# Kernel optimization log

Hardware: AMD Instinct MI355X
Metric: run time of the kernel (lower is better)

The kernel has to match this reference:

```python
import jax, jax.numpy as jnp
import numpy as np

N_NODES = 100000
N_EDGES = 50000
NNZ = 1600000
IN_DIM, HID_DIM, N_CLASSES = 128, 128, 16


def setup_inputs() -> dict:
    key = jax.random.key(0)
    k1, k2, k3, k4, k5 = jax.random.split(key, 5)
    x = jax.random.normal(k1, (N_NODES, IN_DIM), dtype=jnp.float32)
    node_idx = jax.random.randint(k2, (NNZ,), 0, N_NODES, dtype=jnp.int64)
    edge_idx = jax.random.randint(k3, (NNZ,), 0, N_EDGES, dtype=jnp.int64)
    # glorot-ish weights, zero bias (PyG HypergraphConv: Linear(bias=False) + bias Parameter)
    W1 = jax.random.normal(k4, (IN_DIM, HID_DIM), dtype=jnp.float32) * (1.0 / np.sqrt(IN_DIM))
    b1 = jnp.zeros((HID_DIM,), dtype=jnp.float32)
    W2 = jax.random.normal(k5, (HID_DIM, N_CLASSES), dtype=jnp.float32) * (1.0 / np.sqrt(HID_DIM))
    b2 = jnp.zeros((N_CLASSES,), dtype=jnp.float32)
    return {"x": x, "node_idx": node_idx, "edge_idx": edge_idx, "num_edges": N_EDGES,
            "W1": W1, "b1": b1, "W2": W2, "b2": b2}


def hypergraph_conv(x, W, b, node_idx, edge_idx, num_edges):
    """PyG HypergraphConv (no attention, unit hyperedge weights):
       out = D^{-1} H B^{-1} H^T (x W) + b
    implemented as gather -> segment_sum (node->edge) -> gather -> segment_sum (edge->node)."""
    n_nodes = x.shape[0]
    ones = jnp.ones(node_idx.shape[0], dtype=x.dtype)
    deg = jax.ops.segment_sum(ones, node_idx, num_segments=n_nodes)      # D: node degree
    edeg = jax.ops.segment_sum(ones, edge_idx, num_segments=num_edges)   # B: hyperedge size
    Dinv = jnp.where(deg > 0, 1.0 / deg, 0.0)
    Binv = jnp.where(edeg > 0, 1.0 / edeg, 0.0)

    xw = x @ W                                                            # [N, F_out]
    # node -> hyperedge, norm = B^{-1} applied per message (indexed by edge)
    msg_ne = xw[node_idx] * Binv[edge_idx][:, None]                       # [nnz, F_out]
    e_feat = jax.ops.segment_sum(msg_ne, edge_idx, num_segments=num_edges)
    # hyperedge -> node, norm = D^{-1} applied per message (indexed by node)
    msg_en = e_feat[edge_idx] * Dinv[node_idx][:, None]                   # [nnz, F_out]
    out = jax.ops.segment_sum(msg_en, node_idx, num_segments=n_nodes)
    return out + b


def reference(x, node_idx, edge_idx, num_edges, W1, b1, W2, b2):
    # Dropout is inactive in eval mode; model is relu(conv1) -> conv2.
    h = jax.nn.relu(hypergraph_conv(x, W1, b1, node_idx, edge_idx, num_edges))
    return hypergraph_conv(h, W2, b2, node_idx, edge_idx, num_edges)
```

## Files before the change

kernel.cpp:

```cpp
#include <hip/hip_runtime.h>
#include <hip/hip_fp16.h>


#define N_EDGES_C 50000
#define F1 128
#define F2 16
#define CHUNK 4096
#define EBIN_SHIFT 7
#define NBIN_SHIFT 8
#define EBINS 391
#define NBINS 391

typedef __attribute__((ext_vector_type(8))) _Float16 half8;
typedef __attribute__((ext_vector_type(4))) float f32x4;
typedef unsigned short ushort16_t;


__global__ __launch_bounds__(256) void hist_chunk_kernel(
    const int* __restrict__ node_idx, const int* __restrict__ edge_idx,
    int* __restrict__ echunkcnt, int* __restrict__ nchunkcnt, int nnz) {
  __shared__ int ebc[EBINS], nbc[NBINS];
  const int t = threadIdx.x;
  for (int b = t; b < EBINS; b += 256) ebc[b] = 0;
  for (int b = t; b < NBINS; b += 256) nbc[b] = 0;
  __syncthreads();
  const int base = blockIdx.x * CHUNK;
  int end = base + CHUNK; if (end > nnz) end = nnz;
  for (int i = base + t; i < end; i += 256) {
    atomicAdd(&ebc[edge_idx[i] >> EBIN_SHIFT], 1);
    atomicAdd(&nbc[node_idx[i] >> NBIN_SHIFT], 1);
  }
  __syncthreads();
  const int nC = gridDim.x;
  for (int b = t; b < EBINS; b += 256) echunkcnt[b * nC + blockIdx.x] = ebc[b];
  for (int b = t; b < NBINS; b += 256) nchunkcnt[b * nC + blockIdx.x] = nbc[b];
}

__global__ __launch_bounds__(256) void cscan_p1_kernel(
    const int* __restrict__ ecc, const int* __restrict__ ncc,
    int* __restrict__ epart, int* __restrict__ npart,
    int Le, int Ln, int nbE) {
  __shared__ int red[256];
  const int t = threadIdx.x;
  const int b = blockIdx.x;
  const int* src; int L; int* dst; int bb;
  if (b < nbE) { src = ecc; L = Le; dst = epart; bb = b; }
  else         { src = ncc; L = Ln; dst = npart; bb = b - nbE; }
  int base = bb * 1024 + t * 4;
  int s = 0;
#pragma unroll
  for (int j = 0; j < 4; ++j) { int i = base + j; if (i < L) s += src[i]; }
  red[t] = s;
  __syncthreads();
  for (int d = 128; d > 0; d >>= 1) {
    if (t < d) red[t] += red[t + d];
    __syncthreads();
  }
  if (t == 0) dst[bb] = red[0];
}

__global__ __launch_bounds__(256) void cscan_p2_kernel(
    int* __restrict__ epart, int* __restrict__ npart,
    int* __restrict__ ebinbase, int* __restrict__ nbinbase,
    int nbE, int nbN, int nnz) {
  __shared__ int se[256], sn[256];
  const int t = threadIdx.x;
  se[t] = (t < nbE) ? epart[t] : 0;
  sn[t] = (t < nbN) ? npart[t] : 0;
  __syncthreads();
  for (int d = 1; d < 256; d <<= 1) {
    int ve = (t >= d) ? se[t - d] : 0;
    int vn = (t >= d) ? sn[t - d] : 0;
    __syncthreads();
    se[t] += ve; sn[t] += vn;
    __syncthreads();
  }
  if (t < nbE) epart[t] = (t > 0) ? se[t - 1] : 0;
  if (t < nbN) npart[t] = (t > 0) ? sn[t - 1] : 0;
  if (t == 0) { ebinbase[EBINS] = nnz; nbinbase[NBINS] = nnz; }
}

__global__ __launch_bounds__(256) void cscan_p3_kernel(
    const int* __restrict__ ecc, const int* __restrict__ ncc,
    const int* __restrict__ epart, const int* __restrict__ npart,
    int* __restrict__ erunoff, int* __restrict__ nrunoff,
    int* __restrict__ ebinbase, int* __restrict__ nbinbase,
    int Le, int Ln, int nbE, int nC) {
  __shared__ int red[256];
  const int t = threadIdx.x;
  const int b = blockIdx.x;
  const int* src; const int* part; int L; int* ro; int* bba; int bb;
  if (b < nbE) { src = ecc; part = epart; L = Le; ro = erunoff; bba = ebinbase; bb = b; }
  else         { src = ncc; part = npart; L = Ln; ro = nrunoff; bba = nbinbase; bb = b - nbE; }
  int base = bb * 1024 + t * 4;
  int v[4]; int s = 0;
#pragma unroll
  for (int j = 0; j < 4; ++j) { int i = base + j; v[j] = (i < L) ? src[i] : 0; s += v[j]; }
  red[t] = s;
  __syncthreads();
  for (int d = 1; d < 256; d <<= 1) {
    int x = (t >= d) ? red[t - d] : 0;
    __syncthreads();
    red[t] += x;
    __syncthreads();
  }
  int run = part[bb] + ((t > 0) ? red[t - 1] : 0);
#pragma unroll
  for (int j = 0; j < 4; ++j) {
    int i = base + j;
    if (i < L) {
      ro[i] = run;
      if (i % nC == 0) bba[i / nC] = run;
      run += v[j];
    }
  }
}


__global__ __launch_bounds__(256) void stage_kernel(
    const int* __restrict__ node_idx, const int* __restrict__ edge_idx,
    const int* __restrict__ erunoff, const int* __restrict__ nrunoff,
    unsigned* __restrict__ epairs, unsigned* __restrict__ npairs, int nnz) {
  __shared__ int ecur[EBINS], ncur[NBINS];
  const int t = threadIdx.x;
  const int nC = gridDim.x;
  for (int b = t; b < EBINS; b += 256) ecur[b] = erunoff[b * nC + blockIdx.x];
  for (int b = t; b < NBINS; b += 256) ncur[b] = nrunoff[b * nC + blockIdx.x];
  __syncthreads();
  const int base = blockIdx.x * CHUNK;
  int end = base + CHUNK; if (end > nnz) end = nnz;
  for (int i = base + t; i < end; i += 256) {
    int e = edge_idx[i];
    int n = node_idx[i];
    int p = atomicAdd(&ecur[e >> EBIN_SHIFT], 1);
    epairs[p] = ((unsigned)n << 7) | (unsigned)(e & 127);
    int q = atomicAdd(&ncur[n >> NBIN_SHIFT], 1);
    npairs[q] = ((unsigned)e << 8) | (unsigned)(n & 255);
  }
}

__global__ __launch_bounds__(256) void bin_scatter_kernel(
    const unsigned* __restrict__ epairs, const unsigned* __restrict__ npairs,
    const int* __restrict__ ebinbase, const int* __restrict__ nbinbase,
    int* __restrict__ eoff, int* __restrict__ noff,
    int* __restrict__ enbr, ushort16_t* __restrict__ nnbr,
    int n_edges, int n_nodes) {
  __shared__ int cnt[256];
  __shared__ int scn[256];
  const int bid = blockIdx.x;
  const int t = threadIdx.x;
  if (bid < EBINS) {
    const int e0 = bid << EBIN_SHIFT;
    const int ne = min(1 << EBIN_SHIFT, n_edges - e0);
    const int beg = ebinbase[bid], end = ebinbase[bid + 1];
    if (t < 128) cnt[t] = 0;
    __syncthreads();
    for (int j = beg + t; j < end; j += 256) atomicAdd(&cnt[epairs[j] & 127u], 1);
    __syncthreads();
    if (t < 128) scn[t] = cnt[t];
    __syncthreads();
    for (int d = 1; d < 128; d <<= 1) {
      int x = 0;
      if (t < 128 && t >= d) x = scn[t - d];
      __syncthreads();
      if (t < 128) scn[t] += x;
      __syncthreads();
    }
    int pos0 = 0;
    if (t < 128) {
      int excl = (t > 0) ? scn[t - 1] : 0;
      pos0 = beg + excl;
      if (t < ne) eoff[e0 + t] = pos0;
    }
    __syncthreads();
    if (t < 128) scn[t] = pos0;
    __syncthreads();
    for (int j = beg + t; j < end; j += 256) {
      unsigned p = epairs[j];
      int pos = atomicAdd(&scn[p & 127u], 1);
      enbr[pos] = (int)(p >> 7);
    }
    if (bid == EBINS - 1 && t == 0) eoff[n_edges] = end;
  } else {
    const int b = bid - EBINS;
    const int n0 = b << NBIN_SHIFT;
    const int nn = min(1 << NBIN_SHIFT, n_nodes - n0);
    const int beg = nbinbase[b], end = nbinbase[b + 1];
    cnt[t] = 0;
    __syncthreads();
    for (int j = beg + t; j < end; j += 256) atomicAdd(&cnt[npairs[j] & 255u], 1);
    __syncthreads();
    scn[t] = cnt[t];
    __syncthreads();
    for (int d = 1; d < 256; d <<= 1) {
      int x = (t >= d) ? scn[t - d] : 0;
      __syncthreads();
      scn[t] += x;
      __syncthreads();
    }
    int excl = (t > 0) ? scn[t - 1] : 0;
    int pos0 = beg + excl;
    if (t < nn) noff[n0 + t] = pos0;
    __syncthreads();
    scn[t] = pos0;
    __syncthreads();
    for (int j = beg + t; j < end; j += 256) {
      unsigned p = npairs[j];
      int pos = atomicAdd(&scn[p & 255u], 1);
      nnbr[pos] = (ushort16_t)(p >> 8);
    }
    if (bid == EBINS + NBINS - 1 && t == 0) noff[n_nodes] = end;
  }
}


__global__ __launch_bounds__(256) void w1t_kernel(
    const float* __restrict__ W1, __half* __restrict__ W1t) {
  int i = blockIdx.x * 256 + threadIdx.x;
  int n = i >> 7, k = i & 127;
  W1t[i] = __float2half(W1[k * 128 + n]);
}


__global__ __launch_bounds__(256) void gemm1_kernel(
    const float* __restrict__ A, const __half* __restrict__ W1t16,
    __half* __restrict__ C16, int M) {
  __shared__ _Float16 As[64 * 136];
  __shared__ _Float16 Bs[128 * 136];
  const int t = threadIdx.x;
  const int bm = blockIdx.x * 64;

#pragma unroll
  for (int i = 0; i < 8; ++i) {
    int lin = i * 256 + t;
    int row = lin >> 5;
    int c4 = lin & 31;
    int grow = bm + row;
    float4 v = make_float4(0.f, 0.f, 0.f, 0.f);
    if (grow < M) v = *(const float4*)(A + (size_t)grow * 128 + c4 * 4);
    _Float16* dst = &As[row * 136 + c4 * 4];
    dst[0] = (_Float16)v.x; dst[1] = (_Float16)v.y;
    dst[2] = (_Float16)v.z; dst[3] = (_Float16)v.w;
  }
#pragma unroll
  for (int i = 0; i < 8; ++i) {
    int lin = i * 256 + t;
    int n = lin >> 4;
    int c = lin & 15;
    *(float4*)&Bs[n * 136 + c * 8] = *(const float4*)(W1t16 + n * 128 + c * 8);
  }
  __syncthreads();

  const int w = t >> 6;
  const int lane = t & 63;
  const int l16 = lane & 15;
  const int quad = lane >> 4;

  f32x4 acc[8];
#pragma unroll
  for (int n = 0; n < 8; ++n) acc[n] = (f32x4){0.f, 0.f, 0.f, 0.f};

  const _Float16* arow = &As[(w * 16 + l16) * 136 + quad * 8];
#pragma unroll
  for (int kt = 0; kt < 4; ++kt) {
    half8 a = *(const half8*)(arow + kt * 32);
#pragma unroll
    for (int n = 0; n < 8; ++n) {
      half8 b = *(const half8*)&Bs[(n * 16 + l16) * 136 + kt * 32 + quad * 8];
      acc[n] = __builtin_amdgcn_mfma_f32_16x16x32_f16(a, b, acc[n], 0, 0, 0);
    }
  }
  __syncthreads();

#pragma unroll
  for (int n = 0; n < 8; ++n) {
#pragma unroll
    for (int r = 0; r < 4; ++r) {
      int row = w * 16 + quad * 4 + r;
      int col = n * 16 + l16;
      As[row * 136 + col] = (_Float16)acc[n][r];
    }
  }
  __syncthreads();

#pragma unroll
  for (int i = 0; i < 4; ++i) {
    int lin = i * 256 + t;
    int row = lin >> 4;
    int c = lin & 15;
    int grow = bm + row;
    if (grow < M)
      *(float4*)(C16 + (size_t)grow * 128 + c * 8) = *(const float4*)&As[row * 136 + c * 8];
  }
}


__device__ __forceinline__ void acc_mixw(float* ax, f32x4 v, float wt) {
  const unsigned* w = (const unsigned*)&v;
#pragma unroll
  for (int q = 0; q < 4; ++q) {
    asm("v_fma_mix_f32 %0, %1, %2, %0 op_sel:[0,0,0] op_sel_hi:[1,0,0]"
        : "+v"(ax[2 * q]) : "v"(w[q]), "v"(wt));
    asm("v_fma_mix_f32 %0, %1, %2, %0 op_sel:[1,0,0] op_sel_hi:[1,0,0]"
        : "+v"(ax[2 * q + 1]) : "v"(w[q]), "v"(wt));
  }
}

__global__ __launch_bounds__(256) void edge_agg128_kernel(
    const f32x4* __restrict__ feat,
    const int* __restrict__ nbr, const int* __restrict__ off,
    float4* __restrict__ outf, int nseg) {
  int w = (blockIdx.x * 256 + threadIdx.x) >> 6;
  if (w >= nseg) return;
  const int lane = threadIdx.x & 63;
  const int r = lane >> 4;
  const int f = lane & 15;
  int beg = off[w], end = off[w + 1];
  const int kl = end - 1;
  float ax[8];
#pragma unroll
  for (int i = 0; i < 8; ++i) ax[i] = 0.f;
  for (int k = beg + r; k < end; k += 32) {
    int k1 = min(k + 4, kl),  k2 = min(k + 8, kl),  k3 = min(k + 12, kl);
    int k4 = min(k + 16, kl), k5 = min(k + 20, kl), k6 = min(k + 24, kl), k7 = min(k + 28, kl);
    float w1 = (k + 4 <= kl) ? 1.f : 0.f;
    float w2 = (k + 8 <= kl) ? 1.f : 0.f;
    float w3 = (k + 12 <= kl) ? 1.f : 0.f;
    float w4 = (k + 16 <= kl) ? 1.f : 0.f;
    float w5 = (k + 20 <= kl) ? 1.f : 0.f;
    float w6 = (k + 24 <= kl) ? 1.f : 0.f;
    float w7 = (k + 28 <= kl) ? 1.f : 0.f;
    int n0 = nbr[k],  n1 = nbr[k1], n2 = nbr[k2], n3 = nbr[k3];
    int n4 = nbr[k4], n5 = nbr[k5], n6 = nbr[k6], n7 = nbr[k7];
    f32x4 v0 = feat[(size_t)n0 * 16 + f];
    f32x4 v1 = feat[(size_t)n1 * 16 + f];
    f32x4 v2 = feat[(size_t)n2 * 16 + f];
    f32x4 v3 = feat[(size_t)n3 * 16 + f];
    f32x4 v4 = feat[(size_t)n4 * 16 + f];
    f32x4 v5 = feat[(size_t)n5 * 16 + f];
    f32x4 v6 = feat[(size_t)n6 * 16 + f];
    f32x4 v7 = feat[(size_t)n7 * 16 + f];
    asm volatile("" :: "v"(v0), "v"(v1), "v"(v2), "v"(v3),
                       "v"(v4), "v"(v5), "v"(v6), "v"(v7));
    acc_mixw(ax, v0, 1.f); acc_mixw(ax, v1, w1);
    acc_mixw(ax, v2, w2);  acc_mixw(ax, v3, w3);
    acc_mixw(ax, v4, w4);  acc_mixw(ax, v5, w5);
    acc_mixw(ax, v6, w6);  acc_mixw(ax, v7, w7);
  }
#pragma unroll
  for (int i = 0; i < 8; ++i) {
    ax[i] += __shfl_xor(ax[i], 16, 64);
    ax[i] += __shfl_xor(ax[i], 32, 64);
  }
  if (r == 0) {
    float inv = (end > beg) ? 1.f / (float)(end - beg) : 0.f;
    union { float4 f4; __half2 h[4]; } u;
#pragma unroll
    for (int q = 0; q < 4; ++q)
      u.h[q] = __floats2half2_rn(ax[2 * q] * inv, ax[2 * q + 1] * inv);
    outf[(size_t)w * 16 + f] = u.f4;
  }
}

__global__ __launch_bounds__(256) void node_agg128_kernel(
    const f32x4* __restrict__ feat,
    const ushort16_t* __restrict__ nbr, const int* __restrict__ off,
    const float* __restrict__ bias,
    float4* __restrict__ outf, int nseg) {
  int w = (blockIdx.x * 256 + threadIdx.x) >> 6;
  if (w >= nseg) return;
  const int lane = threadIdx.x & 63;
  const int r = lane >> 4;
  const int f = lane & 15;
  int beg = off[w], end = off[w + 1];
  const int kl = end - 1;
  float ax[8];
#pragma unroll
  for (int i = 0; i < 8; ++i) ax[i] = 0.f;
  for (int k = beg + r; k < end; k += 16) {
    int k1 = min(k + 4, kl), k2 = min(k + 8, kl), k3 = min(k + 12, kl);
    float w1 = (k + 4 <= kl) ? 1.f : 0.f;
    float w2 = (k + 8 <= kl) ? 1.f : 0.f;
    float w3 = (k + 12 <= kl) ? 1.f : 0.f;
    int e0 = nbr[k], e1 = nbr[k1], e2 = nbr[k2], e3 = nbr[k3];
    f32x4 v0 = feat[(size_t)e0 * 16 + f];
    f32x4 v1 = feat[(size_t)e1 * 16 + f];
    f32x4 v2 = feat[(size_t)e2 * 16 + f];
    f32x4 v3 = feat[(size_t)e3 * 16 + f];
    asm volatile("" :: "v"(v0), "v"(v1), "v"(v2), "v"(v3));
    acc_mixw(ax, v0, 1.f); acc_mixw(ax, v1, w1);
    acc_mixw(ax, v2, w2);  acc_mixw(ax, v3, w3);
  }
#pragma unroll
  for (int i = 0; i < 8; ++i) {
    ax[i] += __shfl_xor(ax[i], 16, 64);
    ax[i] += __shfl_xor(ax[i], 32, 64);
  }
  if (r == 0) {
    float inv = (end > beg) ? 1.f / (float)(end - beg) : 0.f;
    float4 blo = ((const float4*)bias)[2 * f];
    float4 bhi = ((const float4*)bias)[2 * f + 1];
    float bb[8] = {blo.x, blo.y, blo.z, blo.w, bhi.x, bhi.y, bhi.z, bhi.w};
    union { float4 f4; __half2 h[4]; } u;
#pragma unroll
    for (int q = 0; q < 4; ++q) {
      float hx = fmaxf(ax[2 * q] * inv + bb[2 * q], 0.f);
      float hy = fmaxf(ax[2 * q + 1] * inv + bb[2 * q + 1], 0.f);
      u.h[q] = __floats2half2_rn(hx, hy);
    }
    outf[(size_t)w * 16 + f] = u.f4;
  }
}


__global__ __launch_bounds__(256) void gemm2_kernel(
    const __half* __restrict__ H16, const float* __restrict__ W2,
    __half2* __restrict__ O16, int M) {
  __shared__ float ws2[128 * 16];
  const int t = threadIdx.x;
#pragma unroll
  for (int i = 0; i < 8; ++i) ws2[i * 256 + t] = W2[i * 256 + t];
  __syncthreads();

  int r0 = blockIdx.x * 512 + t;
  int r1 = r0 + 256;
  bool v0 = r0 < M, v1 = r1 < M;
  const __half2* h0 = (const __half2*)(H16 + (size_t)r0 * 128);
  const __half2* h1 = (const __half2*)(H16 + (size_t)r1 * 128);

  float4 acc0[4], acc1[4];
#pragma unroll
  for (int q = 0; q < 4; ++q) {
    acc0[q] = make_float4(0.f, 0.f, 0.f, 0.f);
    acc1[q] = make_float4(0.f, 0.f, 0.f, 0.f);
  }

  for (int k4 = 0; k4 < 32; ++k4) {
    float2 f00 = make_float2(0.f, 0.f), f01 = make_float2(0.f, 0.f);
    float2 f10 = make_float2(0.f, 0.f), f11 = make_float2(0.f, 0.f);
    if (v0) { f00 = __half22float2(h0[2 * k4]); f01 = __half22float2(h0[2 * k4 + 1]); }
    if (v1) { f10 = __half22float2(h1[2 * k4]); f11 = __half22float2(h1[2 * k4 + 1]); }
    const float a0s[4] = {f00.x, f00.y, f01.x, f01.y};
    const float a1s[4] = {f10.x, f10.y, f11.x, f11.y};
#pragma unroll
    for (int j = 0; j < 4; ++j) {
      int k = k4 * 4 + j;
#pragma unroll
      for (int q = 0; q < 4; ++q) {
        float4 b = *(const float4*)&ws2[k * 16 + q * 4];
        acc0[q].x = fmaf(a0s[j], b.x, acc0[q].x);
        acc0[q].y = fmaf(a0s[j], b.y, acc0[q].y);
        acc0[q].z = fmaf(a0s[j], b.z, acc0[q].z);
        acc0[q].w = fmaf(a0s[j], b.w, acc0[q].w);
        acc1[q].x = fmaf(a1s[j], b.x, acc1[q].x);
        acc1[q].y = fmaf(a1s[j], b.y, acc1[q].y);
        acc1[q].z = fmaf(a1s[j], b.z, acc1[q].z);
        acc1[q].w = fmaf(a1s[j], b.w, acc1[q].w);
      }
    }
  }
  if (v0) {
    __half2* op = O16 + (size_t)r0 * 8;
#pragma unroll
    for (int q = 0; q < 4; ++q) {
      op[q * 2]     = __floats2half2_rn(acc0[q].x, acc0[q].y);
      op[q * 2 + 1] = __floats2half2_rn(acc0[q].z, acc0[q].w);
    }
  }
  if (v1) {
    __half2* op = O16 + (size_t)r1 * 8;
#pragma unroll
    for (int q = 0; q < 4; ++q) {
      op[q * 2]     = __floats2half2_rn(acc1[q].x, acc1[q].y);
      op[q * 2 + 1] = __floats2half2_rn(acc1[q].z, acc1[q].w);
    }
  }
}


__global__ __launch_bounds__(256) void edge_agg16_kernel(
    const __half* __restrict__ feat, const int* __restrict__ nbr,
    const int* __restrict__ off, float* __restrict__ outf, int nseg) {
  int gid = blockIdx.x * 256 + threadIdx.x;
  int seg = gid >> 4;
  int c = gid & 15;
  if (seg >= nseg) return;
  int beg = off[seg], end = off[seg + 1];
  float a0 = 0.f, a1 = 0.f, a2 = 0.f, a3 = 0.f;
  int j = beg;
  for (; j + 8 <= end; j += 8) {
    int n0 = nbr[j],     n1 = nbr[j + 1], n2 = nbr[j + 2], n3 = nbr[j + 3];
    int n4 = nbr[j + 4], n5 = nbr[j + 5], n6 = nbr[j + 6], n7 = nbr[j + 7];
    float v0 = __half2float(feat[(size_t)n0 * 16 + c]);
    float v1 = __half2float(feat[(size_t)n1 * 16 + c]);
    float v2 = __half2float(feat[(size_t)n2 * 16 + c]);
    float v3 = __half2float(feat[(size_t)n3 * 16 + c]);
    float v4 = __half2float(feat[(size_t)n4 * 16 + c]);
    float v5 = __half2float(feat[(size_t)n5 * 16 + c]);
    float v6 = __half2float(feat[(size_t)n6 * 16 + c]);
    float v7 = __half2float(feat[(size_t)n7 * 16 + c]);
    a0 += v0 + v4; a1 += v1 + v5; a2 += v2 + v6; a3 += v3 + v7;
  }
  for (; j < end; ++j) a0 += __half2float(feat[(size_t)nbr[j] * 16 + c]);
  float inv = (end > beg) ? 1.f / (float)(end - beg) : 0.f;
  outf[(size_t)seg * 16 + c] = ((a0 + a1) + (a2 + a3)) * inv;
}

__global__ __launch_bounds__(256) void node_agg16_kernel(
    const float* __restrict__ feat, const ushort16_t* __restrict__ nbr,
    const int* __restrict__ off, const float* __restrict__ bias,
    float* __restrict__ outf, int nseg) {
  int gid = blockIdx.x * 256 + threadIdx.x;
  int seg = gid >> 4;
  int c = gid & 15;
  if (seg >= nseg) return;
  int beg = off[seg], end = off[seg + 1];
  float a0 = 0.f, a1 = 0.f, a2 = 0.f, a3 = 0.f;
  int j = beg;
  for (; j + 8 <= end; j += 8) {
    int n0 = nbr[j],     n1 = nbr[j + 1], n2 = nbr[j + 2], n3 = nbr[j + 3];
    int n4 = nbr[j + 4], n5 = nbr[j + 5], n6 = nbr[j + 6], n7 = nbr[j + 7];
    float v0 = feat[(size_t)n0 * 16 + c];
    float v1 = feat[(size_t)n1 * 16 + c];
    float v2 = feat[(size_t)n2 * 16 + c];
    float v3 = feat[(size_t)n3 * 16 + c];
    float v4 = feat[(size_t)n4 * 16 + c];
    float v5 = feat[(size_t)n5 * 16 + c];
    float v6 = feat[(size_t)n6 * 16 + c];
    float v7 = feat[(size_t)n7 * 16 + c];
    a0 += v0 + v4; a1 += v1 + v5; a2 += v2 + v6; a3 += v3 + v7;
  }
  for (; j < end; ++j) a0 += feat[(size_t)nbr[j] * 16 + c];
  float inv = (end > beg) ? 1.f / (float)(end - beg) : 0.f;
  outf[(size_t)seg * 16 + c] = ((a0 + a1) + (a2 + a3)) * inv + bias[c];
}


extern "C" void kernel_launch(void* const* d_in, const int* in_sizes, int n_in,
                              void* d_out, int out_size, void* d_ws, size_t ws_size,
                              hipStream_t stream) {
  const float* x        = (const float*)d_in[0];
  const int*   node_idx = (const int*)d_in[1];
  const int*   edge_idx = (const int*)d_in[2];
  const float* W1 = (const float*)d_in[4];
  const float* b1 = (const float*)d_in[5];
  const float* W2 = (const float*)d_in[6];
  const float* b2 = (const float*)d_in[7];
  float* out = (float*)d_out;

  const int n_nodes = in_sizes[0] / F1;
  const int nnz     = in_sizes[1];
  const int n_edges = N_EDGES_C;
  const int nC      = (nnz + CHUNK - 1) / CHUNK;
  const int Le      = EBINS * nC;
  const int Ln      = NBINS * nC;
  const int nbE     = (Le + 1023) / 1024;
  const int nbN     = (Ln + 1023) / 1024;

  char* ws = (char*)d_ws;
  unsigned* epairs = (unsigned*)(ws + 0);
  unsigned* npairs = (unsigned*)(ws + 6400000);
  __half*  h16    = (__half*)(ws + 0);
  __half*  xw16   = (__half*)(ws + 25600000);
  __half*  ef16   = (__half*)(ws + 51200000);
  __half*  hw216  = (__half*)(ws + 64000000);
  float*   ef2    = (float*)(ws + 70400000);
  int*     enbr   = (int*)(ws + 73600000);
  ushort16_t* nnbr16 = (ushort16_t*)(ws + 80000000);
  int*     eoff   = (int*)(ws + 86400000);
  int*     noff   = (int*)(ws + 86600008);
  int*     echunkcnt = (int*)(ws + 87000016);
  int*     nchunkcnt = (int*)(ws + 87611540);
  int*     erunoff   = (int*)(ws + 88223064);
  int*     nrunoff   = (int*)(ws + 88834588);
  int*     ebinbase  = (int*)(ws + 89446112);
  int*     nbinbase  = (int*)(ws + 89447680);
  int*     epart     = (int*)(ws + 89449248);
  int*     npart     = (int*)(ws + 89450272);
  __half*  w1t16     = (__half*)(ws + 89451520);

  w1t_kernel<<<64, 256, 0, stream>>>(W1, w1t16);

  hist_chunk_kernel<<<nC, 256, 0, stream>>>(node_idx, edge_idx,
                                            echunkcnt, nchunkcnt, nnz);
  cscan_p1_kernel<<<nbE + nbN, 256, 0, stream>>>(echunkcnt, nchunkcnt,
                                                 epart, npart, Le, Ln, nbE);
  cscan_p2_kernel<<<1, 256, 0, stream>>>(epart, npart, ebinbase, nbinbase,
                                         nbE, nbN, nnz);
  cscan_p3_kernel<<<nbE + nbN, 256, 0, stream>>>(echunkcnt, nchunkcnt,
                                                 epart, npart, erunoff, nrunoff,
                                                 ebinbase, nbinbase, Le, Ln, nbE, nC);
  stage_kernel<<<nC, 256, 0, stream>>>(node_idx, edge_idx, erunoff, nrunoff,
                                       epairs, npairs, nnz);
  bin_scatter_kernel<<<EBINS + NBINS, 256, 0, stream>>>(epairs, npairs,
                                                        ebinbase, nbinbase,
                                                        eoff, noff, enbr, nnbr16,
                                                        n_edges, n_nodes);

  gemm1_kernel<<<(n_nodes + 63) / 64, 256, 0, stream>>>(x, w1t16, xw16, n_nodes);
  edge_agg128_kernel<<<(n_edges * 64 + 255) / 256, 256, 0, stream>>>(
      (const f32x4*)xw16, enbr, eoff, (float4*)ef16, n_edges);
  node_agg128_kernel<<<(n_nodes * 64 + 255) / 256, 256, 0, stream>>>(
      (const f32x4*)ef16, nnbr16, noff, b1, (float4*)h16, n_nodes);

  gemm2_kernel<<<(n_nodes + 511) / 512, 256, 0, stream>>>(h16, W2,
                                                          (__half2*)hw216, n_nodes);
  edge_agg16_kernel<<<(n_edges * 16 + 255) / 256, 256, 0, stream>>>(
      hw216, enbr, eoff, ef2, n_edges);
  node_agg16_kernel<<<(n_nodes * 16 + 255) / 256, 256, 0, stream>>>(
      ef2, nnbr16, noff, b2, out, n_nodes);
}
```

Baseline: 355.4 us.

## Replace two-level binned CSR build with global-atomic counting sort

Replaces the chunked histogram plus binned staging and per-bin LDS scatter with direct per-edge/per-node degree counting via global atomics, a scan over the degree arrays, and a global-atomic scatter into the CSR neighbour lists. This removes the intermediate pair arrays and one full read/write pass over them, at the cost of heavy global atomic contention on 150k counters and fully random scatter writes. Neighbour order within each row becomes nondeterministic, which changes floating-point summation order. The degree arrays are zeroed with a memset each call.

```diff
diff --git a/kernel.cpp b/kernel.cpp
--- a/kernel.cpp
+++ b/kernel.cpp
@@ -5,47 +5,33 @@
 #define N_EDGES_C 50000
 #define F1 128
 #define F2 16
-#define CHUNK 4096
-#define EBIN_SHIFT 7
-#define NBIN_SHIFT 8
-#define EBINS 391
-#define NBINS 391
 
 typedef __attribute__((ext_vector_type(8))) _Float16 half8;
 typedef __attribute__((ext_vector_type(4))) float f32x4;
 typedef unsigned short ushort16_t;
 
 
-__global__ __launch_bounds__(256) void hist_chunk_kernel(
+__global__ __launch_bounds__(256) void count_kernel(
     const int* __restrict__ node_idx, const int* __restrict__ edge_idx,
-    int* __restrict__ echunkcnt, int* __restrict__ nchunkcnt, int nnz) {
-  __shared__ int ebc[EBINS], nbc[NBINS];
-  const int t = threadIdx.x;
-  for (int b = t; b < EBINS; b += 256) ebc[b] = 0;
-  for (int b = t; b < NBINS; b += 256) nbc[b] = 0;
-  __syncthreads();
-  const int base = blockIdx.x * CHUNK;
-  int end = base + CHUNK; if (end > nnz) end = nnz;
-  for (int i = base + t; i < end; i += 256) {
-    atomicAdd(&ebc[edge_idx[i] >> EBIN_SHIFT], 1);
-    atomicAdd(&nbc[node_idx[i] >> NBIN_SHIFT], 1);
-  }
-  __syncthreads();
-  const int nC = gridDim.x;
-  for (int b = t; b < EBINS; b += 256) echunkcnt[b * nC + blockIdx.x] = ebc[b];
-  for (int b = t; b < NBINS; b += 256) nchunkcnt[b * nC + blockIdx.x] = nbc[b];
-}
-
-__global__ __launch_bounds__(256) void cscan_p1_kernel(
-    const int* __restrict__ ecc, const int* __restrict__ ncc,
+    int* __restrict__ edeg, int* __restrict__ ndeg, int nnz) {
+  int i = blockIdx.x * 256 + threadIdx.x;
+  const int stride = gridDim.x * 256;
+  for (; i < nnz; i += stride) {
+    atomicAdd(&edeg[edge_idx[i]], 1);
+    atomicAdd(&ndeg[node_idx[i]], 1);
+  }
+}
+
+__global__ __launch_bounds__(256) void scan_p1_kernel(
+    const int* __restrict__ edeg, const int* __restrict__ ndeg,
     int* __restrict__ epart, int* __restrict__ npart,
     int Le, int Ln, int nbE) {
   __shared__ int red[256];
   const int t = threadIdx.x;
   const int b = blockIdx.x;
   const int* src; int L; int* dst; int bb;
-  if (b < nbE) { src = ecc; L = Le; dst = epart; bb = b; }
-  else         { src = ncc; L = Ln; dst = npart; bb = b - nbE; }
+  if (b < nbE) { src = edeg; L = Le; dst = epart; bb = b; }
+  else         { src = ndeg; L = Ln; dst = npart; bb = b - nbE; }
   int base = bb * 1024 + t * 4;
   int s = 0;
 #pragma unroll
@@ -59,10 +45,10 @@
   if (t == 0) dst[bb] = red[0];
 }
 
-__global__ __launch_bounds__(256) void cscan_p2_kernel(
+__global__ __launch_bounds__(256) void scan_p2_kernel(
     int* __restrict__ epart, int* __restrict__ npart,
-    int* __restrict__ ebinbase, int* __restrict__ nbinbase,
-    int nbE, int nbN, int nnz) {
+    int* __restrict__ eoff, int* __restrict__ noff,
+    int nbE, int nbN, int n_edges, int n_nodes, int nnz) {
   __shared__ int se[256], sn[256];
   const int t = threadIdx.x;
   se[t] = (t < nbE) ? epart[t] : 0;
@@ -77,21 +63,21 @@
   }
   if (t < nbE) epart[t] = (t > 0) ? se[t - 1] : 0;
   if (t < nbN) npart[t] = (t > 0) ? sn[t - 1] : 0;
-  if (t == 0) { ebinbase[EBINS] = nnz; nbinbase[NBINS] = nnz; }
-}
-
-__global__ __launch_bounds__(256) void cscan_p3_kernel(
-    const int* __restrict__ ecc, const int* __restrict__ ncc,
+  if (t == 0) { eoff[n_edges] = nnz; noff[n_nodes] = nnz; }
+}
+
+__global__ __launch_bounds__(256) void scan_p3_kernel(
+    const int* __restrict__ edeg, const int* __restrict__ ndeg,
     const int* __restrict__ epart, const int* __restrict__ npart,
-    int* __restrict__ erunoff, int* __restrict__ nrunoff,
-    int* __restrict__ ebinbase, int* __restrict__ nbinbase,
-    int Le, int Ln, int nbE, int nC) {
+    int* __restrict__ eoff, int* __restrict__ noff,
+    int* __restrict__ ecur, int* __restrict__ ncur,
+    int Le, int Ln, int nbE) {
   __shared__ int red[256];
   const int t = threadIdx.x;
   const int b = blockIdx.x;
-  const int* src; const int* part; int L; int* ro; int* bba; int bb;
-  if (b < nbE) { src = ecc; part = epart; L = Le; ro = erunoff; bba = ebinbase; bb = b; }
-  else         { src = ncc; part = npart; L = Ln; ro = nrunoff; bba = nbinbase; bb = b - nbE; }
+  const int* src; const int* part; int L; int* off; int* cur; int bb;
+  if (b < nbE) { src = edeg; part = epart; L = Le; off = eoff; cur = ecur; bb = b; }
+  else         { src = ndeg; part = npart; L = Ln; off = noff; cur = ncur; bb = b - nbE; }
   int base = bb * 1024 + t * 4;
   int v[4]; int s = 0;
 #pragma unroll
@@ -109,107 +95,26 @@
   for (int j = 0; j < 4; ++j) {
     int i = base + j;
     if (i < L) {
-      ro[i] = run;
-      if (i % nC == 0) bba[i / nC] = run;
+      off[i] = run;
+      cur[i] = run;
       run += v[j];
     }
   }
 }
 
-
-__global__ __launch_bounds__(256) void stage_kernel(
+__global__ __launch_bounds__(256) void scatter_kernel(
     const int* __restrict__ node_idx, const int* __restrict__ edge_idx,
-    const int* __restrict__ erunoff, const int* __restrict__ nrunoff,
-    unsigned* __restrict__ epairs, unsigned* __restrict__ npairs, int nnz) {
-  __shared__ int ecur[EBINS], ncur[NBINS];
-  const int t = threadIdx.x;
-  const int nC = gridDim.x;
-  for (int b = t; b < EBINS; b += 256) ecur[b] = erunoff[b * nC + blockIdx.x];
-  for (int b = t; b < NBINS; b += 256) ncur[b] = nrunoff[b * nC + blockIdx.x];
-  __syncthreads();
-  const int base = blockIdx.x * CHUNK;
-  int end = base + CHUNK; if (end > nnz) end = nnz;
-  for (int i = base + t; i < end; i += 256) {
+    int* __restrict__ ecur, int* __restrict__ ncur,
+    int* __restrict__ enbr, ushort16_t* __restrict__ nnbr, int nnz) {
+  int i = blockIdx.x * 256 + threadIdx.x;
+  const int stride = gridDim.x * 256;
+  for (; i < nnz; i += stride) {
     int e = edge_idx[i];
     int n = node_idx[i];
-    int p = atomicAdd(&ecur[e >> EBIN_SHIFT], 1);
-    epairs[p] = ((unsigned)n << 7) | (unsigned)(e & 127);
-    int q = atomicAdd(&ncur[n >> NBIN_SHIFT], 1);
-    npairs[q] = ((unsigned)e << 8) | (unsigned)(n & 255);
-  }
-}
-
-__global__ __launch_bounds__(256) void bin_scatter_kernel(
-    const unsigned* __restrict__ epairs, const unsigned* __restrict__ npairs,
-    const int* __restrict__ ebinbase, const int* __restrict__ nbinbase,
-    int* __restrict__ eoff, int* __restrict__ noff,
-    int* __restrict__ enbr, ushort16_t* __restrict__ nnbr,
-    int n_edges, int n_nodes) {
-  __shared__ int cnt[256];
-  __shared__ int scn[256];
-  const int bid = blockIdx.x;
-  const int t = threadIdx.x;
-  if (bid < EBINS) {
-    const int e0 = bid << EBIN_SHIFT;
-    const int ne = min(1 << EBIN_SHIFT, n_edges - e0);
-    const int beg = ebinbase[bid], end = ebinbase[bid + 1];
-    if (t < 128) cnt[t] = 0;
-    __syncthreads();
-    for (int j = beg + t; j < end; j += 256) atomicAdd(&cnt[epairs[j] & 127u], 1);
-    __syncthreads();
-    if (t < 128) scn[t] = cnt[t];
-    __syncthreads();
-    for (int d = 1; d < 128; d <<= 1) {
-      int x = 0;
-      if (t < 128 && t >= d) x = scn[t - d];
-      __syncthreads();
-      if (t < 128) scn[t] += x;
-      __syncthreads();
-    }
-    int pos0 = 0;
-    if (t < 128) {
-      int excl = (t > 0) ? scn[t - 1] : 0;
-      pos0 = beg + excl;
-      if (t < ne) eoff[e0 + t] = pos0;
-    }
-    __syncthreads();
-    if (t < 128) scn[t] = pos0;
-    __syncthreads();
-    for (int j = beg + t; j < end; j += 256) {
-      unsigned p = epairs[j];
-      int pos = atomicAdd(&scn[p & 127u], 1);
-      enbr[pos] = (int)(p >> 7);
-    }
-    if (bid == EBINS - 1 && t == 0) eoff[n_edges] = end;
-  } else {
-    const int b = bid - EBINS;
-    const int n0 = b << NBIN_SHIFT;
-    const int nn = min(1 << NBIN_SHIFT, n_nodes - n0);
-    const int beg = nbinbase[b], end = nbinbase[b + 1];
-    cnt[t] = 0;
-    __syncthreads();
-    for (int j = beg + t; j < end; j += 256) atomicAdd(&cnt[npairs[j] & 255u], 1);
-    __syncthreads();
-    scn[t] = cnt[t];
-    __syncthreads();
-    for (int d = 1; d < 256; d <<= 1) {
-      int x = (t >= d) ? scn[t - d] : 0;
-      __syncthreads();
-      scn[t] += x;
-      __syncthreads();
-    }
-    int excl = (t > 0) ? scn[t - 1] : 0;
-    int pos0 = beg + excl;
-    if (t < nn) noff[n0 + t] = pos0;
-    __syncthreads();
-    scn[t] = pos0;
-    __syncthreads();
-    for (int j = beg + t; j < end; j += 256) {
-      unsigned p = npairs[j];
-      int pos = atomicAdd(&scn[p & 255u], 1);
-      nnbr[pos] = (ushort16_t)(p >> 8);
-    }
-    if (bid == EBINS + NBINS - 1 && t == 0) noff[n_nodes] = end;
+    int p = atomicAdd(&ecur[e], 1);
+    enbr[p] = n;
+    int q = atomicAdd(&ncur[n], 1);
+    nnbr[q] = (ushort16_t)e;
   }
 }
 
@@ -551,15 +456,10 @@
   const int n_nodes = in_sizes[0] / F1;
   const int nnz     = in_sizes[1];
   const int n_edges = N_EDGES_C;
-  const int nC      = (nnz + CHUNK - 1) / CHUNK;
-  const int Le      = EBINS * nC;
-  const int Ln      = NBINS * nC;
-  const int nbE     = (Le + 1023) / 1024;
-  const int nbN     = (Ln + 1023) / 1024;
+  const int nbE     = (n_edges + 1023) / 1024;
+  const int nbN     = (n_nodes + 1023) / 1024;
 
   char* ws = (char*)d_ws;
-  unsigned* epairs = (unsigned*)(ws + 0);
-  unsigned* npairs = (unsigned*)(ws + 6400000);
   __half*  h16    = (__half*)(ws + 0);
   __half*  xw16   = (__half*)(ws + 25600000);
   __half*  ef16   = (__half*)(ws + 51200000);
@@ -569,33 +469,26 @@
   ushort16_t* nnbr16 = (ushort16_t*)(ws + 80000000);
   int*     eoff   = (int*)(ws + 86400000);
   int*     noff   = (int*)(ws + 86600008);
-  int*     echunkcnt = (int*)(ws + 87000016);
-  int*     nchunkcnt = (int*)(ws + 87611540);
-  int*     erunoff   = (int*)(ws + 88223064);
-  int*     nrunoff   = (int*)(ws + 88834588);
-  int*     ebinbase  = (int*)(ws + 89446112);
-  int*     nbinbase  = (int*)(ws + 89447680);
-  int*     epart     = (int*)(ws + 89449248);
-  int*     npart     = (int*)(ws + 89450272);
-  __half*  w1t16     = (__half*)(ws + 89451520);
-
+  int*     edeg   = (int*)(ws + 87000016);
+  int*     ndeg   = (int*)(ws + 87200016);
+  int*     ecur   = (int*)(ws + 87600016);
+  int*     ncur   = (int*)(ws + 87800016);
+  int*     epart  = (int*)(ws + 88200016);
+  int*     npart  = (int*)(ws + 88201040);
+  __half*  w1t16  = (__half*)(ws + 88202064);
+
+  hipMemsetAsync(edeg, 0, 600000, stream);
   w1t_kernel<<<64, 256, 0, stream>>>(W1, w1t16);
-
-  hist_chunk_kernel<<<nC, 256, 0, stream>>>(node_idx, edge_idx,
-                                            echunkcnt, nchunkcnt, nnz);
-  cscan_p1_kernel<<<nbE + nbN, 256, 0, stream>>>(echunkcnt, nchunkcnt,
-                                                 epart, npart, Le, Ln, nbE);
-  cscan_p2_kernel<<<1, 256, 0, stream>>>(epart, npart, ebinbase, nbinbase,
-                                         nbE, nbN, nnz);
-  cscan_p3_kernel<<<nbE + nbN, 256, 0, stream>>>(echunkcnt, nchunkcnt,
-                                                 epart, npart, erunoff, nrunoff,
-                                                 ebinbase, nbinbase, Le, Ln, nbE, nC);
-  stage_kernel<<<nC, 256, 0, stream>>>(node_idx, edge_idx, erunoff, nrunoff,
-                                       epairs, npairs, nnz);
-  bin_scatter_kernel<<<EBINS + NBINS, 256, 0, stream>>>(epairs, npairs,
-                                                        ebinbase, nbinbase,
-                                                        eoff, noff, enbr, nnbr16,
-                                                        n_edges, n_nodes);
+  count_kernel<<<2048, 256, 0, stream>>>(node_idx, edge_idx, edeg, ndeg, nnz);
+  scan_p1_kernel<<<nbE + nbN, 256, 0, stream>>>(edeg, ndeg, epart, npart,
+                                                n_edges, n_nodes, nbE);
+  scan_p2_kernel<<<1, 256, 0, stream>>>(epart, npart, eoff, noff,
+                                        nbE, nbN, n_edges, n_nodes, nnz);
+  scan_p3_kernel<<<nbE + nbN, 256, 0, stream>>>(edeg, ndeg, epart, npart,
+                                                eoff, noff, ecur, ncur,
+                                                n_edges, n_nodes, nbE);
+  scatter_kernel<<<2048, 256, 0, stream>>>(node_idx, edge_idx, ecur, ncur,
+                                           enbr, nnbr16, nnz);
 
   gemm1_kernel<<<(n_nodes + 63) / 64, 256, 0, stream>>>(x, w1t16, xw16, n_nodes);
   edge_agg128_kernel<<<(n_edges * 64 + 255) / 256, 256, 0, stream>>>(
```

Result: slower. 701.0 us (+97.2%).
